# Kernel tuning notes

Hardware: AMD Instinct MI355X
Metric: run time of the kernel (lower is better)

The kernel has to match this reference:

```python
import jax, jax.numpy as jnp
import numpy as np

N_ENT, N_REL, DIM = 100000, 500, 128
B, F = 256, 20000


def setup_inputs() -> dict:
    key = jax.random.key(0)
    ks = jax.random.split(key, 8)
    return {
        "ent_emb": jax.random.normal(ks[0], (N_ENT, DIM), jnp.float32),
        "rel_emb": jax.random.normal(ks[1], (N_REL, DIM), jnp.float32),
        "heads": jax.random.randint(ks[2], (B,), 0, N_ENT, jnp.int64),
        "rels": jax.random.randint(ks[3], (B,), 0, N_REL, jnp.int64),
        "tails": jax.random.randint(ks[4], (B,), 0, N_ENT, jnp.int64),
        "f_heads": jax.random.randint(ks[5], (F,), 0, N_ENT, jnp.int64),
        "f_rels": jax.random.randint(ks[6], (F,), 0, N_REL, jnp.int64),
        "f_tails": jax.random.randint(ks[7], (F,), 0, N_ENT, jnp.int64),
    }


def _all_scores(ent_emb, rel_emb, heads, rels, tails):
    # TransE L2 score: s(h,r,t) = -||e_h + e_r - e_t||_2
    e_h, e_r, e_t = ent_emb[heads], rel_emb[rels], ent_emb[tails]
    eps = 1e-12
    triple_score = -jnp.sqrt(jnp.maximum(jnp.sum((e_h + e_r - e_t) ** 2, -1), eps))  # [B]
    ent_sq = jnp.sum(ent_emb ** 2, -1)  # [N]
    # head corruption: score(n, r, t) = -||e_n + (e_r - e_t)||
    q = e_r - e_t  # [B, d]
    head_sq = ent_sq[None, :] + 2.0 * jnp.einsum("bd,nd->bn", q, ent_emb) + jnp.sum(q ** 2, -1)[:, None]
    head_scores = -jnp.sqrt(jnp.maximum(head_sq, eps))  # [B, N]
    # tail corruption: score(h, r, n) = -||e_n - (e_h + e_r)||
    p = e_h + e_r  # [B, d]
    tail_sq = ent_sq[None, :] - 2.0 * jnp.einsum("bd,nd->bn", p, ent_emb) + jnp.sum(p ** 2, -1)[:, None]
    tail_scores = -jnp.sqrt(jnp.maximum(tail_sq, eps))  # [B, N]
    return triple_score, head_scores, tail_scores


def _filter_masks(heads, rels, tails, f_heads, f_rels, f_tails, n_ent):
    # mask[b, n] = True iff corrupted triple is in the filter set (to be excluded)
    b = heads.shape[0]
    rows = jnp.arange(b)[:, None]  # [B, 1]
    # head corruption filtered where (f_rel == r_b) & (f_tail == t_b): exclude f_head
    match_h = (f_rels[None, :] == rels[:, None]) & (f_tails[None, :] == tails[:, None])  # [B, F]
    head_mask = jnp.zeros((b, n_ent), bool).at[rows, f_heads[None, :]].max(match_h)
    # tail corruption filtered where (f_rel == r_b) & (f_head == h_b): exclude f_tail
    match_t = (f_rels[None, :] == rels[:, None]) & (f_heads[None, :] == heads[:, None])
    tail_mask = jnp.zeros((b, n_ent), bool).at[rows, f_tails[None, :]].max(match_t)
    return head_mask, tail_mask


def reference(ent_emb, rel_emb, heads, rels, tails, f_heads, f_rels, f_tails):
    triple_score, head_scores, tail_scores = _all_scores(ent_emb, rel_emb, heads, rels, tails)
    head_mask, tail_mask = _filter_masks(heads, rels, tails, f_heads, f_rels, f_tails, ent_emb.shape[0])
    neg_inf = jnp.float32(-jnp.inf)
    head_scores = jnp.where(head_mask, neg_inf, head_scores)
    tail_scores = jnp.where(tail_mask, neg_inf, tail_scores)
    head_ranks = jnp.sum((head_scores > triple_score[:, None]).astype(jnp.int32), axis=1) + 1
    tail_ranks = jnp.sum((tail_scores > triple_score[:, None]).astype(jnp.int32), axis=1) + 1
    return head_ranks, tail_ranks
```

## Files before the change

### kernel.cpp

```cpp
#include <hip/hip_runtime.h>
#include <cstdint>
#include <cstddef>

#define N_ENT 100000
#define DIM 128
#define BSZ 256
#define FSZ 20000
#define BM 64
#define NBT 1563
#define NPAD (NBT * 64)
#define MCAP_B 64

typedef __attribute__((ext_vector_type(8))) short bf16x8;
typedef __attribute__((ext_vector_type(4))) float f32x4;

#define KEEP(x) asm volatile("" : "+v"(x))

#define WS_QALL   0
#define WS_QSQ    262144
#define WS_THR    264192
#define WS_THC    266240
#define WS_CNT    268288
#define WS_PERCNT 270336
#define WS_MATCH  271360
#define WS_QBF    402432
#define WS_QBFP   533504
#define WS_PART   664576
#define WS_ESQH   2265088
#define WS_ABF    2665216
#define WS_NEED   (WS_ABF + (size_t)NPAD * DIM * 2)

__device__ inline unsigned short f2bf(float x) {
    union { float f; uint32_t u; } v; v.f = x;
    uint32_t u = v.u;
    u += 0x7fffu + ((u >> 16) & 1);
    return (unsigned short)(u >> 16);
}

__global__ __launch_bounds__(256) void k_front(
    const float* __restrict__ ent, const float* __restrict__ rel,
    const int* __restrict__ heads, const int* __restrict__ rels, const int* __restrict__ tails,
    const int* __restrict__ fh, const int* __restrict__ fr, const int* __restrict__ ft,
    float* __restrict__ qall, float* __restrict__ qsq, float* __restrict__ thr,
    float* __restrict__ thc, int* __restrict__ cnt,
    unsigned short* __restrict__ qbf, unsigned short* __restrict__ qbfp,
    unsigned short* __restrict__ abf, float* __restrict__ esqh,
    int* __restrict__ percnt, int2* __restrict__ match)
{
    int bid = blockIdx.x;
    int tid = threadIdx.x;

    if (bid < NBT) {
        int k4 = tid & 31;
        int ks = k4 >> 3, kq = (k4 >> 1) & 3, e0 = (k4 & 1) * 4;
        int base4 = bid * 2048;
        #pragma unroll
        for (int i = 0; i < 8; i++) {
            int fidx = base4 + i * 256 + tid;
            int np = fidx >> 5;
            bool valid = np < N_ENT;
            float4 u = make_float4(0.f, 0.f, 0.f, 0.f);
            if (valid) u = ((const float4*)ent)[fidx];
            float ss = u.x * u.x + u.y * u.y + u.z * u.z + u.w * u.w;
            ss += __shfl_xor(ss, 1);
            ss += __shfl_xor(ss, 2);
            ss += __shfl_xor(ss, 4);
            ss += __shfl_xor(ss, 8);
            ss += __shfl_xor(ss, 16);
            if (k4 == 0) esqh[np] = valid ? 0.5f * ss : 1.5e38f;
            uint2 w;
            w.x = (uint32_t)f2bf(u.x) | ((uint32_t)f2bf(u.y) << 16);
            w.y = (uint32_t)f2bf(u.z) | ((uint32_t)f2bf(u.w) << 16);
            int t = np >> 4;
            size_t idx = ((size_t)(t * 4 + ks) * 64 + kq * 16 + (np & 15)) * 8 + e0;
            *(uint2*)(abf + idx) = w;
        }
        return;
    }

    if (bid < NBT + BSZ) {
        if (tid >= 64) return;
        int b = bid - NBT;
        int h = heads[b], r = rels[b], t = tails[b];
        float s0 = 0.f, s1 = 0.f, s2 = 0.f;
        #pragma unroll
        for (int half = 0; half < 2; half++) {
            int d = tid + half * 64;
            float eh = ent[(size_t)h * DIM + d];
            float er = rel[(size_t)r * DIM + d];
            float et = ent[(size_t)t * DIM + d];
            float diff = eh + er - et;
            float q = er - et;
            float p = eh + er;
            qall[(size_t)b * DIM + d] = q;
            qall[(size_t)(BSZ + b) * DIM + d] = -p;
            unsigned short qb16 = f2bf(q), pb16 = f2bf(-p);
            qbf[(size_t)b * DIM + d] = qb16;
            qbf[(size_t)(BSZ + b) * DIM + d] = pb16;
            int ks = d >> 5, kq = (d >> 3) & 3, e = d & 7;
            int l0 = kq * 16 + (b & 15);
            int c0 = b >> 4, c1 = (BSZ + b) >> 4;
            qbfp[(size_t)((c0 * 4 + ks) * 64 + l0) * 8 + e] = qb16;
            qbfp[(size_t)((c1 * 4 + ks) * 64 + l0) * 8 + e] = pb16;
            s0 += diff * diff; s1 += q * q; s2 += p * p;
        }
        #pragma unroll
        for (int off = 32; off; off >>= 1) {
            s0 += __shfl_xor(s0, off);
            s1 += __shfl_xor(s1, off);
            s2 += __shfl_xor(s2, off);
        }
        if (tid == 0) {
            float th = fmaxf(s0, 1e-12f);
            thr[b] = th; thr[BSZ + b] = th;
            qsq[b] = s1; qsq[BSZ + b] = s2;
            thc[b] = (th - s1) * 0.5f;
            thc[BSZ + b] = (th - s2) * 0.5f;
            cnt[b] = 0;  cnt[BSZ + b] = 0;
        }
        return;
    }

    {
        int b = bid - NBT - BSZ;
        __shared__ int nm;
        if (tid == 0) nm = 0;
        __syncthreads();
        int k1b = rels[b] * 100000 + tails[b];
        int k2b = rels[b] * 100000 + heads[b];
        for (int f = tid; f < FSZ; f += 256) {
            int vr = fr[f], vt = ft[f], vh = fh[f];
            int fk1 = vr * 100000 + vt;
            int fk2 = vr * 100000 + vh;
            if (fk1 == k1b) {
                int p = atomicAdd(&nm, 1);
                if (p < MCAP_B) match[b * MCAP_B + p] = make_int2(0, vh);
            }
            if (fk2 == k2b) {
                int p = atomicAdd(&nm, 1);
                if (p < MCAP_B) match[b * MCAP_B + p] = make_int2(1, vt);
            }
        }
        __syncthreads();
        if (tid == 0) percnt[b] = nm < MCAP_B ? nm : MCAP_B;
    }
}

__global__ __launch_bounds__(256, 2) void k_count(
    const unsigned short* __restrict__ abf, const float* __restrict__ esqh,
    const unsigned short* __restrict__ qbfp, const float* __restrict__ thc,
    unsigned short* __restrict__ part)
{
    int tid = threadIdx.x;
    int l = tid & 63;
    int bt = blockIdx.x * 4 + (tid >> 6);
    if (bt >= NBT) return;

    bf16x8 a[4][4];
    #pragma unroll
    for (int s = 0; s < 4; s++)
        #pragma unroll
        for (int ks = 0; ks < 4; ks++) {
            a[s][ks] = *(const bf16x8*)(abf + ((size_t)((4 * bt + s) * 4 + ks) * 64 + l) * 8);
            KEEP(a[s][ks]);
        }
    f32x4 ehv[4];
    #pragma unroll
    for (int s = 0; s < 4; s++) {
        #pragma unroll
        for (int r = 0; r < 4; r++)
            ehv[s][r] = esqh[bt * BM + s * 16 + (l >> 4) * 4 + r];
        KEEP(ehv[s]);
    }

    bf16x8 bcur[4], bn1[4], bn2[4];
    #pragma unroll
    for (int ks = 0; ks < 4; ks++) {
        bcur[ks] = *(const bf16x8*)(qbfp + ((size_t)(0 * 4 + ks) * 64 + l) * 8);
        bn1[ks]  = *(const bf16x8*)(qbfp + ((size_t)(1 * 4 + ks) * 64 + l) * 8);
    }
    float tc  = thc[l & 15];
    float tn1 = thc[16 + (l & 15)];
    float tn2;

    uint32_t creg[8] = {0, 0, 0, 0, 0, 0, 0, 0};

    #pragma unroll
    for (int c = 0; c < 32; c++) {
        if (c < 30) {
            #pragma unroll
            for (int ks = 0; ks < 4; ks++)
                bn2[ks] = *(const bf16x8*)(qbfp + ((size_t)((c + 2) * 4 + ks) * 64 + l) * 8);
            tn2 = thc[(c + 2) * 16 + (l & 15)];
        }
        f32x4 acc[4];
        #pragma unroll
        for (int s = 0; s < 4; s++)
            acc[s] = __builtin_amdgcn_mfma_f32_16x16x32_bf16(a[s][0], bcur[0], ehv[s], 0, 0, 0);
        #pragma unroll
        for (int ks = 1; ks < 4; ks++)
            #pragma unroll
            for (int s = 0; s < 4; s++)
                acc[s] = __builtin_amdgcn_mfma_f32_16x16x32_bf16(a[s][ks], bcur[ks], acc[s], 0, 0, 0);
        uint32_t cl = 0;
        #pragma unroll
        for (int s = 0; s < 4; s++)
            #pragma unroll
            for (int r = 0; r < 4; r++)
                cl += (acc[s][r] < tc) ? 1u : 0u;
        creg[c >> 2] += cl << (8 * (c & 3));
        tc = tn1; tn1 = tn2;
        #pragma unroll
        for (int ks = 0; ks < 4; ks++) { bcur[ks] = bn1[ks]; bn1[ks] = bn2[ks]; }
    }

    #pragma unroll
    for (int i = 0; i < 8; i++) {
        uint32_t x = creg[i];
        x += __shfl_xor(x, 16);
        x += __shfl_xor(x, 32);
        creg[i] = x;
    }
    if (l < 16) {
        #pragma unroll
        for (int c = 0; c < 32; c++)
            part[(size_t)bt * 512 + c * 16 + l] =
                (unsigned short)((creg[c >> 2] >> (8 * (c & 3))) & 0xffu);
    }
}

__global__ __launch_bounds__(128, 3) void k_count_fb(
    const float* __restrict__ ent,
    const unsigned short* __restrict__ qbf,
    const float* __restrict__ thc,
    int* __restrict__ cnt)
{
    int tid = threadIdx.x;
    int lane = tid & 63, wave = tid >> 6;
    int base = blockIdx.x * BM;
    int koff = (lane >> 4) * 8;
    int colq = wave * 256 + (lane & 15);
    const unsigned short* qb = qbf + (size_t)colq * DIM + koff;
    bf16x8 bcur[4], bnext[4];
    #pragma unroll
    for (int ks = 0; ks < 4; ks++) bcur[ks] = *(const bf16x8*)(qb + ks * 32);
    bf16x8 a[4][4];
    float hsq[4];
    #pragma unroll
    for (int s = 0; s < 4; s++) {
        int n = base + s * 16 + (lane & 15);
        bool valid = n < N_ENT;
        const float* rowp = ent + (size_t)(valid ? n : (N_ENT - 1)) * DIM + koff;
        float ss = 0.f;
        #pragma unroll
        for (int ks = 0; ks < 4; ks++) {
            float4 u0 = *(const float4*)(rowp + ks * 32);
            float4 u1 = *(const float4*)(rowp + ks * 32 + 4);
            ss += u0.x*u0.x + u0.y*u0.y + u0.z*u0.z + u0.w*u0.w
                + u1.x*u1.x + u1.y*u1.y + u1.z*u1.z + u1.w*u1.w;
            bf16x8 f;
            f[0]=(short)f2bf(u0.x); f[1]=(short)f2bf(u0.y); f[2]=(short)f2bf(u0.z); f[3]=(short)f2bf(u0.w);
            f[4]=(short)f2bf(u1.x); f[5]=(short)f2bf(u1.y); f[6]=(short)f2bf(u1.z); f[7]=(short)f2bf(u1.w);
            a[s][ks] = f; KEEP(a[s][ks]);
        }
        ss += __shfl_xor(ss, 16); ss += __shfl_xor(ss, 32);
        hsq[s] = valid ? ss * 0.5f : 1.5e38f;
    }
    float eh[4][4];
    #pragma unroll
    for (int s = 0; s < 4; s++)
        #pragma unroll
        for (int r = 0; r < 4; r++) { eh[s][r] = __shfl(hsq[s], (lane >> 4) * 4 + r); KEEP(eh[s][r]); }
    #pragma unroll
    for (int c = 0; c < 16; c++) {
        if (c < 15) {
            #pragma unroll
            for (int ks = 0; ks < 4; ks++)
                bnext[ks] = *(const bf16x8*)(qb + (size_t)(c + 1) * 16 * DIM + ks * 32);
        }
        float tcv = thc[colq + c * 16];
        f32x4 acc[4];
        #pragma unroll
        for (int s = 0; s < 4; s++) acc[s] = (f32x4){0.f, 0.f, 0.f, 0.f};
        #pragma unroll
        for (int ks = 0; ks < 4; ks++)
            #pragma unroll
            for (int s = 0; s < 4; s++)
                acc[s] = __builtin_amdgcn_mfma_f32_16x16x32_bf16(a[s][ks], bcur[ks], acc[s], 0, 0, 0);
        int cl = 0;
        #pragma unroll
        for (int s = 0; s < 4; s++)
            #pragma unroll
            for (int r = 0; r < 4; r++)
                cl += (acc[s][r] < tcv - eh[s][r]) ? 1 : 0;
        cl += __shfl_xor(cl, 16);
        cl += __shfl_xor(cl, 32);
        if (lane < 16) atomicAdd(&cnt[colq + c * 16], cl);
        #pragma unroll
        for (int ks = 0; ks < 4; ks++) bcur[ks] = bnext[ks];
    }
}

__global__ __launch_bounds__(256) void k_adjust(
    const float* __restrict__ ent,
    const float* __restrict__ qall, const float* __restrict__ qsq, const float* __restrict__ thr,
    const int* __restrict__ cnt, const unsigned short* __restrict__ part, int use_part,
    const int* __restrict__ percnt, const int2* __restrict__ match,
    int* __restrict__ out)
{
    int key = blockIdx.x;
    int side = key >> 8, b = key & 255;
    int tid = threadIdx.x;
    __shared__ int ids[MCAP_B];
    __shared__ int nm;
    __shared__ int wsum[4];
    if (tid == 0) nm = 0;
    __syncthreads();

    int acc = 0;
    if (use_part) {
        for (int i = tid; i < NBT; i += 256)
            acc += part[(size_t)i * 512 + key];
    } else if (tid == 0) {
        acc = cnt[key];
    }

    int M = percnt[b];
    if (tid < M) {
        int2 e = match[b * MCAP_B + tid];
        if (e.x == side) { int p = atomicAdd(&nm, 1); ids[p] = e.y; }
    }
    __syncthreads();
    int mm = nm;
    const float* qv = qall + (size_t)key * DIM;
    float qq = qsq[key], th = thr[key];
    for (int i = tid; i < mm; i += 256) {
        int id = ids[i];
        bool dup = false;
        for (int j = 0; j < i; j++) if (ids[j] == id) { dup = true; break; }
        if (!dup) {
            const float* en = ent + (size_t)id * DIM;
            float es = 0.f, dot = 0.f;
            for (int d = 0; d < DIM; d++) { float x = en[d]; es += x * x; dot += x * qv[d]; }
            if (fmaxf(es + 2.f * dot + qq, 1e-12f) < th) acc--;
        }
    }
    #pragma unroll
    for (int off = 32; off; off >>= 1) acc += __shfl_xor(acc, off);
    int lane = tid & 63, wv = tid >> 6;
    if (lane == 0) wsum[wv] = acc;
    __syncthreads();
    if (tid == 0) out[key] = wsum[0] + wsum[1] + wsum[2] + wsum[3] + 1;
}

extern "C" void kernel_launch(void* const* d_in, const int* in_sizes, int n_in,
                              void* d_out, int out_size, void* d_ws, size_t ws_size,
                              hipStream_t stream)
{
    const float* ent   = (const float*)d_in[0];
    const float* rel   = (const float*)d_in[1];
    const int*   heads = (const int*)d_in[2];
    const int*   rels  = (const int*)d_in[3];
    const int*   tails = (const int*)d_in[4];
    const int*   fh    = (const int*)d_in[5];
    const int*   fr    = (const int*)d_in[6];
    const int*   ft    = (const int*)d_in[7];
    int* out = (int*)d_out;

    char* ws = (char*)d_ws;
    float* qall = (float*)(ws + WS_QALL);
    float* qsq  = (float*)(ws + WS_QSQ);
    float* thr  = (float*)(ws + WS_THR);
    float* thc  = (float*)(ws + WS_THC);
    int*   cnt  = (int*)(ws + WS_CNT);
    int*   percnt = (int*)(ws + WS_PERCNT);
    int2*  match  = (int2*)(ws + WS_MATCH);
    unsigned short* qbf   = (unsigned short*)(ws + WS_QBF);
    unsigned short* qbfp  = (unsigned short*)(ws + WS_QBFP);
    unsigned short* part  = (unsigned short*)(ws + WS_PART);
    float* esqh = (float*)(ws + WS_ESQH);
    unsigned short* abf  = (unsigned short*)(ws + WS_ABF);

    int use_part = (ws_size >= (size_t)WS_NEED) ? 1 : 0;

    k_front<<<NBT + 2 * BSZ, 256, 0, stream>>>(ent, rel, heads, rels, tails, fh, fr, ft,
                                               qall, qsq, thr, thc, cnt, qbf, qbfp,
                                               abf, esqh, percnt, match);
    if (use_part)
        k_count<<<(NBT + 3) / 4, 256, 0, stream>>>(abf, esqh, qbfp, thc, part);
    else
        k_count_fb<<<NBT, 128, 0, stream>>>(ent, qbf, thc, cnt);
    k_adjust<<<2 * BSZ, 256, 0, stream>>>(ent, qall, qsq, thr, cnt, part, use_part,
                                          percnt, match, out);
}
```

Measured before the change: 62.42 us.

## Fuse entity bf16 conversion and norm computation into the counting kernel

The pre-pass in k_front that converted all entity embeddings to a bf16 MFMA-swizzled buffer and wrote half squared norms is removed. k_count now loads fp32 rows directly from the entity table, computes squared norms with shuffles, and converts to bf16 fragments in registers. This avoids writing and re-reading about 25MB of intermediate bf16 data and shrinks k_front. In exchange, k_count reads twice the bytes per element, uses less-coalesced strided fp32 loads, and carries extra conversion ALU work.

After: 58.04 us. 7.0% less time.

```diff
diff --git a/kernel.cpp b/kernel.cpp
--- a/kernel.cpp
+++ b/kernel.cpp
@@ -8,7 +8,6 @@
 #define FSZ 20000
 #define BM 64
 #define NBT 1563
-#define NPAD (NBT * 64)
 #define MCAP_B 64
 
 typedef __attribute__((ext_vector_type(8))) short bf16x8;
@@ -26,9 +25,7 @@
 #define WS_QBF    402432
 #define WS_QBFP   533504
 #define WS_PART   664576
-#define WS_ESQH   2265088
-#define WS_ABF    2665216
-#define WS_NEED   (WS_ABF + (size_t)NPAD * DIM * 2)
+#define WS_NEED   (WS_PART + NBT * 512 * 2)
 
 __device__ inline unsigned short f2bf(float x) {
     union { float f; uint32_t u; } v; v.f = x;
@@ -44,85 +41,13 @@
     float* __restrict__ qall, float* __restrict__ qsq, float* __restrict__ thr,
     float* __restrict__ thc, int* __restrict__ cnt,
     unsigned short* __restrict__ qbf, unsigned short* __restrict__ qbfp,
-    unsigned short* __restrict__ abf, float* __restrict__ esqh,
     int* __restrict__ percnt, int2* __restrict__ match)
 {
     int bid = blockIdx.x;
     int tid = threadIdx.x;
 
-    if (bid < NBT) {
-        int k4 = tid & 31;
-        int ks = k4 >> 3, kq = (k4 >> 1) & 3, e0 = (k4 & 1) * 4;
-        int base4 = bid * 2048;
-        #pragma unroll
-        for (int i = 0; i < 8; i++) {
-            int fidx = base4 + i * 256 + tid;
-            int np = fidx >> 5;
-            bool valid = np < N_ENT;
-            float4 u = make_float4(0.f, 0.f, 0.f, 0.f);
-            if (valid) u = ((const float4*)ent)[fidx];
-            float ss = u.x * u.x + u.y * u.y + u.z * u.z + u.w * u.w;
-            ss += __shfl_xor(ss, 1);
-            ss += __shfl_xor(ss, 2);
-            ss += __shfl_xor(ss, 4);
-            ss += __shfl_xor(ss, 8);
-            ss += __shfl_xor(ss, 16);
-            if (k4 == 0) esqh[np] = valid ? 0.5f * ss : 1.5e38f;
-            uint2 w;
-            w.x = (uint32_t)f2bf(u.x) | ((uint32_t)f2bf(u.y) << 16);
-            w.y = (uint32_t)f2bf(u.z) | ((uint32_t)f2bf(u.w) << 16);
-            int t = np >> 4;
-            size_t idx = ((size_t)(t * 4 + ks) * 64 + kq * 16 + (np & 15)) * 8 + e0;
-            *(uint2*)(abf + idx) = w;
-        }
-        return;
-    }
-
-    if (bid < NBT + BSZ) {
-        if (tid >= 64) return;
-        int b = bid - NBT;
-        int h = heads[b], r = rels[b], t = tails[b];
-        float s0 = 0.f, s1 = 0.f, s2 = 0.f;
-        #pragma unroll
-        for (int half = 0; half < 2; half++) {
-            int d = tid + half * 64;
-            float eh = ent[(size_t)h * DIM + d];
-            float er = rel[(size_t)r * DIM + d];
-            float et = ent[(size_t)t * DIM + d];
-            float diff = eh + er - et;
-            float q = er - et;
-            float p = eh + er;
-            qall[(size_t)b * DIM + d] = q;
-            qall[(size_t)(BSZ + b) * DIM + d] = -p;
-            unsigned short qb16 = f2bf(q), pb16 = f2bf(-p);
-            qbf[(size_t)b * DIM + d] = qb16;
-            qbf[(size_t)(BSZ + b) * DIM + d] = pb16;
-            int ks = d >> 5, kq = (d >> 3) & 3, e = d & 7;
-            int l0 = kq * 16 + (b & 15);
-            int c0 = b >> 4, c1 = (BSZ + b) >> 4;
-            qbfp[(size_t)((c0 * 4 + ks) * 64 + l0) * 8 + e] = qb16;
-            qbfp[(size_t)((c1 * 4 + ks) * 64 + l0) * 8 + e] = pb16;
-            s0 += diff * diff; s1 += q * q; s2 += p * p;
-        }
-        #pragma unroll
-        for (int off = 32; off; off >>= 1) {
-            s0 += __shfl_xor(s0, off);
-            s1 += __shfl_xor(s1, off);
-            s2 += __shfl_xor(s2, off);
-        }
-        if (tid == 0) {
-            float th = fmaxf(s0, 1e-12f);
-            thr[b] = th; thr[BSZ + b] = th;
-            qsq[b] = s1; qsq[BSZ + b] = s2;
-            thc[b] = (th - s1) * 0.5f;
-            thc[BSZ + b] = (th - s2) * 0.5f;
-            cnt[b] = 0;  cnt[BSZ + b] = 0;
-        }
-        return;
-    }
-
-    {
-        int b = bid - NBT - BSZ;
+    if (bid < BSZ) {
+        int b = bid;
         __shared__ int nm;
         if (tid == 0) nm = 0;
         __syncthreads();
@@ -143,11 +68,52 @@
         }
         __syncthreads();
         if (tid == 0) percnt[b] = nm < MCAP_B ? nm : MCAP_B;
+        return;
+    }
+
+    if (tid >= 64) return;
+    int b = bid - BSZ;
+    int h = heads[b], r = rels[b], t = tails[b];
+    float s0 = 0.f, s1 = 0.f, s2 = 0.f;
+    #pragma unroll
+    for (int half = 0; half < 2; half++) {
+        int d = tid + half * 64;
+        float eh = ent[(size_t)h * DIM + d];
+        float er = rel[(size_t)r * DIM + d];
+        float et = ent[(size_t)t * DIM + d];
+        float diff = eh + er - et;
+        float q = er - et;
+        float p = eh + er;
+        qall[(size_t)b * DIM + d] = q;
+        qall[(size_t)(BSZ + b) * DIM + d] = -p;
+        unsigned short qb16 = f2bf(q), pb16 = f2bf(-p);
+        qbf[(size_t)b * DIM + d] = qb16;
+        qbf[(size_t)(BSZ + b) * DIM + d] = pb16;
+        int ks = d >> 5, kq = (d >> 3) & 3, e = d & 7;
+        int l0 = kq * 16 + (b & 15);
+        int c0 = b >> 4, c1 = (BSZ + b) >> 4;
+        qbfp[(size_t)((c0 * 4 + ks) * 64 + l0) * 8 + e] = qb16;
+        qbfp[(size_t)((c1 * 4 + ks) * 64 + l0) * 8 + e] = pb16;
+        s0 += diff * diff; s1 += q * q; s2 += p * p;
+    }
+    #pragma unroll
+    for (int off = 32; off; off >>= 1) {
+        s0 += __shfl_xor(s0, off);
+        s1 += __shfl_xor(s1, off);
+        s2 += __shfl_xor(s2, off);
+    }
+    if (tid == 0) {
+        float th = fmaxf(s0, 1e-12f);
+        thr[b] = th; thr[BSZ + b] = th;
+        qsq[b] = s1; qsq[BSZ + b] = s2;
+        thc[b] = (th - s1) * 0.5f;
+        thc[BSZ + b] = (th - s2) * 0.5f;
+        cnt[b] = 0;  cnt[BSZ + b] = 0;
     }
 }
 
 __global__ __launch_bounds__(256, 2) void k_count(
-    const unsigned short* __restrict__ abf, const float* __restrict__ esqh,
+    const float* __restrict__ ent,
     const unsigned short* __restrict__ qbfp, const float* __restrict__ thc,
     unsigned short* __restrict__ part)
 {
@@ -155,23 +121,37 @@
     int l = tid & 63;
     int bt = blockIdx.x * 4 + (tid >> 6);
     if (bt >= NBT) return;
+    int koff = (l >> 4) * 8;
 
     bf16x8 a[4][4];
+    float hsq[4];
+    #pragma unroll
+    for (int s = 0; s < 4; s++) {
+        int n = bt * BM + s * 16 + (l & 15);
+        bool valid = n < N_ENT;
+        const float* rowp = ent + (size_t)(valid ? n : (N_ENT - 1)) * DIM + koff;
+        float ss = 0.f;
+        #pragma unroll
+        for (int ks = 0; ks < 4; ks++) {
+            float4 u0 = *(const float4*)(rowp + ks * 32);
+            float4 u1 = *(const float4*)(rowp + ks * 32 + 4);
+            ss += u0.x*u0.x + u0.y*u0.y + u0.z*u0.z + u0.w*u0.w
+                + u1.x*u1.x + u1.y*u1.y + u1.z*u1.z + u1.w*u1.w;
+            bf16x8 f;
+            f[0]=(short)f2bf(u0.x); f[1]=(short)f2bf(u0.y); f[2]=(short)f2bf(u0.z); f[3]=(short)f2bf(u0.w);
+            f[4]=(short)f2bf(u1.x); f[5]=(short)f2bf(u1.y); f[6]=(short)f2bf(u1.z); f[7]=(short)f2bf(u1.w);
+            a[s][ks] = f;
+        }
+        ss += __shfl_xor(ss, 16);
+        ss += __shfl_xor(ss, 32);
+        hsq[s] = valid ? ss * 0.5f : 1.5e38f;
+    }
+    f32x4 ehv[4];
     #pragma unroll
     for (int s = 0; s < 4; s++)
         #pragma unroll
-        for (int ks = 0; ks < 4; ks++) {
-            a[s][ks] = *(const bf16x8*)(abf + ((size_t)((4 * bt + s) * 4 + ks) * 64 + l) * 8);
-            KEEP(a[s][ks]);
-        }
-    f32x4 ehv[4];
-    #pragma unroll
-    for (int s = 0; s < 4; s++) {
-        #pragma unroll
         for (int r = 0; r < 4; r++)
-            ehv[s][r] = esqh[bt * BM + s * 16 + (l >> 4) * 4 + r];
-        KEEP(ehv[s]);
-    }
+            ehv[s][r] = __shfl(hsq[s], (l >> 4) * 4 + r);
 
     bf16x8 bcur[4], bn1[4], bn2[4];
     #pragma unroll
@@ -187,6 +167,12 @@
 
     #pragma unroll
     for (int c = 0; c < 32; c++) {
+        #pragma unroll
+        for (int s = 0; s < 4; s++) {
+            KEEP(ehv[s]);
+            #pragma unroll
+            for (int ks = 0; ks < 4; ks++) KEEP(a[s][ks]);
+        }
         if (c < 30) {
             #pragma unroll
             for (int ks = 0; ks < 4; ks++)
@@ -378,16 +364,14 @@
     unsigned short* qbf   = (unsigned short*)(ws + WS_QBF);
     unsigned short* qbfp  = (unsigned short*)(ws + WS_QBFP);
     unsigned short* part  = (unsigned short*)(ws + WS_PART);
-    float* esqh = (float*)(ws + WS_ESQH);
-    unsigned short* abf  = (unsigned short*)(ws + WS_ABF);
 
     int use_part = (ws_size >= (size_t)WS_NEED) ? 1 : 0;
 
-    k_front<<<NBT + 2 * BSZ, 256, 0, stream>>>(ent, rel, heads, rels, tails, fh, fr, ft,
-                                               qall, qsq, thr, thc, cnt, qbf, qbfp,
-                                               abf, esqh, percnt, match);
+    k_front<<<2 * BSZ, 256, 0, stream>>>(ent, rel, heads, rels, tails, fh, fr, ft,
+                                         qall, qsq, thr, thc, cnt, qbf, qbfp,
+                                         percnt, match);
     if (use_part)
-        k_count<<<(NBT + 3) / 4, 256, 0, stream>>>(abf, esqh, qbfp, thc, part);
+        k_count<<<(NBT + 3) / 4, 256, 0, stream>>>(ent, qbfp, thc, part);
     else
         k_count_fb<<<NBT, 128, 0, stream>>>(ent, qbf, thc, cnt);
     k_adjust<<<2 * BSZ, 256, 0, stream>>>(ent, qall, qsq, thr, cnt, part, use_part,
```
